# Optimization experiments

Hardware: AMD Instinct MI355X
Metric: run time of the kernel (lower is better)

## Reference

```python
import jax, jax.numpy as jnp
import numpy as np

B, T, C = 4, 2048, 512
H, CDR_HEADS = 8, 2
D = C // H


def setup_inputs() -> dict:
    key = jax.random.key(0)
    ks = jax.random.split(key, 12)
    s = 1.0 / np.sqrt(C)
    return {
        "x": jax.random.normal(ks[0], (B, T, C), dtype=jnp.float32),
        "mask": jax.random.randint(ks[1], (B, T), 0, 2, dtype=jnp.int32),
        "cdrs_score": jax.random.randint(ks[2], (B, T), 0, 2, dtype=jnp.int32),
        "Wq": jax.random.normal(ks[3], (C, C), dtype=jnp.float32) * s,
        "bq": jnp.zeros((C,), dtype=jnp.float32),
        "Wk": jax.random.normal(ks[4], (C, C), dtype=jnp.float32) * s,
        "bk": jnp.zeros((C,), dtype=jnp.float32),
        "Wv": jax.random.normal(ks[5], (C, C), dtype=jnp.float32) * s,
        "bv": jnp.zeros((C,), dtype=jnp.float32),
        "Wo": jax.random.normal(ks[6], (C, C), dtype=jnp.float32) * s,
        "bo": jnp.zeros((C,), dtype=jnp.float32),
    }


def reference(x, mask, cdrs_score, Wq, bq, Wk, bk, Wv, bv, Wo, bo):
    # projections -> [B, H, T, D]
    def heads(y):
        return y.reshape(B, T, H, D).transpose(0, 2, 1, 3)

    q = heads(x @ Wq + bq)
    k = heads(x @ Wk + bk)
    v = heads(x @ Wv + bv)

    scores = jnp.einsum("bhqd,bhkd->bhqk", q, k) / jnp.sqrt(jnp.float32(D))

    # padding mask: keys with mask==0 are invalid for all heads
    pad = (mask == 0)[:, None, None, :]                      # [B,1,1,T]
    scores = jnp.where(pad, -jnp.inf, scores)

    # CDR key mask for the first CDR_HEADS heads; disabled if a sample has no CDR tokens
    cdr_key_mask = (cdrs_score == 0)                          # [B, T]
    all_masked = jnp.all(cdr_key_mask, axis=-1, keepdims=True)  # [B, 1]
    cdr_key_mask = jnp.where(all_masked, False, cdr_key_mask)   # [B, T]
    head_is_cdr = (jnp.arange(H) < CDR_HEADS)[None, :, None, None]  # [1,H,1,1]
    cdr_full = head_is_cdr & cdr_key_mask[:, None, None, :]         # [B,H,1,T]
    scores = jnp.where(cdr_full, -jnp.inf, scores)

    attn = jax.nn.softmax(scores, axis=-1)                    # [B,H,T,T]
    ctx = jnp.einsum("bhqk,bhkd->bhqd", attn, v)
    ctx = ctx.transpose(0, 2, 1, 3).reshape(B, T, C)
    return ctx @ Wo + bo
```

## Files before the change

kernel.cpp:

```cpp
#include <hip/hip_runtime.h>
#include <math.h>

#define B_ 4
#define T_ 2048
#define C_ 512
#define H_ 8
#define D_ 64
#define CDR_HEADS_ 2
#define NROWS (B_ * T_)

typedef unsigned short ush;
typedef __bf16  bf16x8 __attribute__((ext_vector_type(8)));
typedef float   f32x4  __attribute__((ext_vector_type(4)));

#define MFMA16(a, b, c) __builtin_amdgcn_mfma_f32_16x16x32_bf16((a), (b), (c), 0, 0, 0)

static __device__ __forceinline__ ush f2bf(float f) {
    unsigned u = __float_as_uint(f);
    u += 0x7FFF + ((u >> 16) & 1);
    return (ush)(u >> 16);
}
static __device__ __forceinline__ float bf2f(ush h) {
    return __uint_as_float(((unsigned)h) << 16);
}

static __device__ __forceinline__ void gload16(const void* gsrc, void* ldst) {
    __builtin_amdgcn_global_load_lds(
        (const __attribute__((address_space(1))) unsigned int*)gsrc,
        (__attribute__((address_space(3))) unsigned int*)ldst, 16, 0, 0);
}

__global__ __launch_bounds__(256) void prep_kernel(
    const float* __restrict__ x,
    const float* __restrict__ W0, const float* __restrict__ W1,
    const float* __restrict__ W2, const float* __restrict__ W3,
    const int* __restrict__ mask, const int* __restrict__ cdrs,
    ush* __restrict__ Xh, ush* __restrict__ Xl,
    ush* __restrict__ Wth, ush* __restrict__ Wtl,
    int* __restrict__ klist, int* __restrict__ kcnt) {
    __shared__ int s_any;
    __shared__ int sa[256], sb[256];
    const int bid = blockIdx.x, tid = threadIdx.x;

    if (bid < 2048) {
        const int id = bid * 256 + tid;
        const int m = id >> 6, kc = id & 63;
        const float* p = x + (size_t)m * C_ + kc * 8;
        const float4 a = ((const float4*)p)[0];
        const float4 b2 = ((const float4*)p)[1];
        float xv[8] = {a.x, a.y, a.z, a.w, b2.x, b2.y, b2.z, b2.w};
        union { ush u[8]; int4 q; } hi, lo;
#pragma unroll
        for (int i = 0; i < 8; ++i) {
            const ush h = f2bf(xv[i]);
            hi.u[i] = h;
            lo.u[i] = f2bf(xv[i] - bf2f(h));
        }
        const int mt = m >> 7, ml = m & 127, kt = kc >> 2, cidx = kc & 3;
        const size_t tbase = ((size_t)mt * 16 + kt) * 4096;
        const int boff = ml * 64 + ((cidx ^ ((ml >> 1) & 3)) << 4);
        *(int4*)((char*)(Xh + tbase) + boff) = hi.q;
        *(int4*)((char*)(Xl + tbase) + boff) = lo.q;
    } else if (bid < 2560) {
        const int z = bid - 2048;
        const int mat = z >> 7;
        const float* W = (mat == 0) ? W0 : (mat == 1) ? W1 : (mat == 2) ? W2 : W3;
        const int id = (z & 127) * 256 + tid;
        const int n = id & 511, kc = id >> 9;
        float xv[8];
#pragma unroll
        for (int j = 0; j < 8; ++j)
            xv[j] = W[(size_t)(kc * 8 + j) * C_ + n];
        union { ush u[8]; int4 q; } hi, lo;
#pragma unroll
        for (int i = 0; i < 8; ++i) {
            const ush h = f2bf(xv[i]);
            hi.u[i] = h;
            lo.u[i] = f2bf(xv[i] - bf2f(h));
        }
        const int nt = n >> 7, nl = n & 127, kt = kc >> 2, cidx = kc & 3;
        const size_t tbase = (size_t)mat * 262144 + ((size_t)nt * 16 + kt) * 4096;
        const int boff = nl * 64 + ((cidx ^ ((nl >> 1) & 3)) << 4);
        *(int4*)((char*)(Wth + tbase) + boff) = hi.q;
        *(int4*)((char*)(Wtl + tbase) + boff) = lo.q;
    } else {
        const int b = bid - 2560;
        if (tid == 0) s_any = 0;
        __syncthreads();
        int m8[8], c8[8];
        int any = 0, ca = 0;
        const int base = b * T_ + tid * 8;
#pragma unroll
        for (int i = 0; i < 8; ++i) {
            m8[i] = mask[base + i];
            c8[i] = cdrs[base + i];
            any |= c8[i];
            ca += (m8[i] != 0);
        }
        if (any) s_any = 1;
        __syncthreads();
        const int en = s_any;
        int cb = 0;
#pragma unroll
        for (int i = 0; i < 8; ++i)
            cb += (m8[i] != 0 && (!en || c8[i] != 0));
        sa[tid] = ca; sb[tid] = cb;
        __syncthreads();
        for (int off = 1; off < 256; off <<= 1) {
            int va = 0, vb = 0;
            if (tid >= off) { va = sa[tid - off]; vb = sb[tid - off]; }
            __syncthreads();
            sa[tid] += va; sb[tid] += vb;
            __syncthreads();
        }
        int offA = sa[tid] - ca;
        int offB = sb[tid] - cb;
        int* la = klist + (size_t)(b * 2 + 0) * T_;
        int* lb = klist + (size_t)(b * 2 + 1) * T_;
#pragma unroll
        for (int i = 0; i < 8; ++i) {
            const int t = tid * 8 + i;
            if (m8[i] != 0) la[offA++] = t;
            if (m8[i] != 0 && (!en || c8[i] != 0)) lb[offB++] = t;
        }
        if (tid == 255) {
            kcnt[b * 2 + 0] = sa[255];
            kcnt[b * 2 + 1] = sb[255];
        }
    }
}

template <int OUTMODE>
static __device__ __forceinline__ void gemm3_body(
    const ush* __restrict__ Ah_g, const ush* __restrict__ Al_g,
    const ush* __restrict__ Bh_g, const ush* __restrict__ Bl_g,
    const float* __restrict__ bias, void* __restrict__ outp, float scale) {
    __shared__ char lds[32768];
    char* const sAh = lds;
    char* const sAl = lds + 8192;
    char* const sBh = lds + 16384;
    char* const sBl = lds + 24576;

    const int tid = threadIdx.x;
    const int lane = tid & 63, w = tid >> 6;
    const int g = lane >> 4, l15 = lane & 15;
    const int wr = w >> 1, wc = w & 1;
    const int mt = blockIdx.x, nt = blockIdx.y;

    const char* gAh = (const char*)Ah_g + (size_t)(mt * 16) * 8192;
    const char* gAl = (const char*)Al_g + (size_t)(mt * 16) * 8192;
    const char* gBh = (const char*)Bh_g + (size_t)(nt * 16) * 8192;
    const char* gBl = (const char*)Bl_g + (size_t)(nt * 16) * 8192;

    f32x4 acc[4][4];
#pragma unroll
    for (int i = 0; i < 4; ++i)
#pragma unroll
        for (int j = 0; j < 4; ++j)
#pragma unroll
            for (int r = 0; r < 4; ++r) acc[i][j][r] = 0.f;

    const int lw = w * 2048;
    for (int kt = 0; kt < 16; ++kt) {
        __syncthreads();
        const size_t gb = (size_t)kt * 8192 + lw + lane * 16;
        gload16(gAh + gb,        sAh + lw);
        gload16(gAh + gb + 1024, sAh + lw + 1024);
        gload16(gAl + gb,        sAl + lw);
        gload16(gAl + gb + 1024, sAl + lw + 1024);
        gload16(gBh + gb,        sBh + lw);
        gload16(gBh + gb + 1024, sBh + lw + 1024);
        gload16(gBl + gb,        sBl + lw);
        gload16(gBl + gb + 1024, sBl + lw + 1024);
        __syncthreads();

        bf16x8 fah[4], fal[4], fbh[4], fbl[4];
#pragma unroll
        for (int rb = 0; rb < 4; ++rb) {
            const int row = wr * 64 + rb * 16 + l15;
            const int off = row * 64 + ((g ^ ((row >> 1) & 3)) << 4);
            fah[rb] = __builtin_bit_cast(bf16x8, *(const int4*)(sAh + off));
            fal[rb] = __builtin_bit_cast(bf16x8, *(const int4*)(sAl + off));
        }
#pragma unroll
        for (int cb = 0; cb < 4; ++cb) {
            const int row = wc * 64 + cb * 16 + l15;
            const int off = row * 64 + ((g ^ ((row >> 1) & 3)) << 4);
            fbh[cb] = __builtin_bit_cast(bf16x8, *(const int4*)(sBh + off));
            fbl[cb] = __builtin_bit_cast(bf16x8, *(const int4*)(sBl + off));
        }
#pragma unroll
        for (int rb = 0; rb < 4; ++rb)
#pragma unroll
            for (int cb = 0; cb < 4; ++cb) {
                acc[rb][cb] = MFMA16(fah[rb], fbh[cb], acc[rb][cb]);
                acc[rb][cb] = MFMA16(fah[rb], fbl[cb], acc[rb][cb]);
                acc[rb][cb] = MFMA16(fal[rb], fbh[cb], acc[rb][cb]);
            }
    }

    const int mbase = mt * 128 + wr * 64;
    const int nbase = nt * 128 + wc * 64;
    float bcol[4];
#pragma unroll
    for (int cb = 0; cb < 4; ++cb) bcol[cb] = bias[nbase + cb * 16 + l15];

#pragma unroll
    for (int rb = 0; rb < 4; ++rb)
#pragma unroll
        for (int cb = 0; cb < 4; ++cb) {
            const int colg = nbase + cb * 16 + l15;
#pragma unroll
            for (int r = 0; r < 4; ++r) {
                const int m = mbase + rb * 16 + g * 4 + r;
                const float vv = acc[rb][cb][r] + bcol[cb];
                if (OUTMODE == 0) {
                    ((float*)outp)[(size_t)m * C_ + colg] = vv;
                } else {
                    const int bb = m >> 11, t = m & (T_ - 1);
                    const int h = colg >> 6, d = colg & 63;
                    ((ush*)outp)[(((size_t)(bb * H_ + h) * T_ + t) * D_) + d] =
                        f2bf(vv * scale);
                }
            }
        }
}

__global__ __launch_bounds__(256) void gemm3_qkv_kernel(
    const ush* __restrict__ Xh, const ush* __restrict__ Xl,
    const ush* __restrict__ Wth, const ush* __restrict__ Wtl,
    const float* __restrict__ bq, const float* __restrict__ bk,
    const float* __restrict__ bv,
    ush* __restrict__ Qb, ush* __restrict__ Kb, ush* __restrict__ Vb) {
    const int z = blockIdx.z;
    const ush* bh = Wth + (size_t)z * 262144;
    const ush* bl = Wtl + (size_t)z * 262144;
    if (z == 0)      gemm3_body<1>(Xh, Xl, bh, bl, bq, Qb, 0.125f);
    else if (z == 1) gemm3_body<1>(Xh, Xl, bh, bl, bk, Kb, 1.0f);
    else             gemm3_body<1>(Xh, Xl, bh, bl, bv, Vb, 1.0f);
}

__global__ __launch_bounds__(256) void gemm3_out_kernel(
    const ush* __restrict__ Ch, const ush* __restrict__ Cl,
    const ush* __restrict__ Wth, const ush* __restrict__ Wtl,
    const float* __restrict__ bo, float* __restrict__ out) {
    gemm3_body<0>(Ch, Cl, Wth + (size_t)3 * 262144, Wtl + (size_t)3 * 262144,
                  bo, out, 1.0f);
}

__global__ __launch_bounds__(256) void gather_kernel(
    const ush* __restrict__ Kb, const ush* __restrict__ Vb,
    const int* __restrict__ klist, const int* __restrict__ kcnt,
    ush* __restrict__ Kc, ush* __restrict__ Vct) {
    __shared__ ush Vs[64 * 72];
    const int tid = threadIdx.x;
    const int ti = blockIdx.x, h = blockIdx.y, b = blockIdx.z;
    const int sel = (h < CDR_HEADS_) ? 1 : 0;
    const int NV = kcnt[b * 2 + sel];
    if (ti * 64 >= NV) return;
    const int* __restrict__ list = klist + (size_t)(b * 2 + sel) * T_;
    const size_t bh = (size_t)b * H_ + h;
    const ush* kb_ = Kb + bh * T_ * D_;
    const ush* vb_ = Vb + bh * T_ * D_;
    ush* kt = Kc + bh * (32 * 4096) + (size_t)ti * 4096;
    ush* vt = Vct + bh * (32 * 4096) + (size_t)ti * 4096;

    const int i = tid >> 2, c = tid & 3;
    const int pos = ti * 64 + i;
    int4 kv0 = {0,0,0,0}, kv1 = {0,0,0,0}, vv0 = {0,0,0,0}, vv1 = {0,0,0,0};
    if (pos < NV) {
        const int row = list[pos];
        const int4* kr = (const int4*)(kb_ + (size_t)row * D_ + c * 16);
        kv0 = kr[0]; kv1 = kr[1];
        const int4* vr = (const int4*)(vb_ + (size_t)row * D_ + c * 16);
        vv0 = vr[0]; vv1 = vr[1];
    }
    {
        const int s0 = (c * 2) ^ (i & 7), s1 = (c * 2 + 1) ^ (i & 7);
        *(int4*)(kt + i * 64 + s0 * 8) = kv0;
        *(int4*)(kt + i * 64 + s1 * 8) = kv1;
    }
    *(int4*)(Vs + i * 72 + c * 16)     = vv0;
    *(int4*)(Vs + i * 72 + c * 16 + 8) = vv1;
    __syncthreads();
    {
        const int d = tid >> 2, c2 = tid & 3;
        union { ush u[16]; int4 q[2]; } pk;
#pragma unroll
        for (int ii = 0; ii < 16; ++ii)
            pk.u[ii] = Vs[(c2 * 16 + ii) * 72 + d];
        const int s0 = (c2 * 2) ^ (d & 7), s1 = (c2 * 2 + 1) ^ (d & 7);
        *(int4*)(vt + d * 64 + s0 * 8) = pk.q[0];
        *(int4*)(vt + d * 64 + s1 * 8) = pk.q[1];
    }
}

__global__ __launch_bounds__(512) void attn_mfma_kernel(
    const ush* __restrict__ Qb, const ush* __restrict__ Kc,
    const ush* __restrict__ Vct, const int* __restrict__ kcnt,
    ush* __restrict__ Xh, ush* __restrict__ Xl) {
    __shared__ ush Ks[2][4096];
    __shared__ ush Vts[2][4096];
    __shared__ ush Pl[8192];

    const int tid = threadIdx.x;
    const int lane = tid & 63, w = tid >> 6;
    const int g = lane >> 4, l15 = lane & 15;

    const int i = blockIdx.x;
    const int x7 = i & 7, local = i >> 3;
    const int b = local >> 4;
    const int h = (x7 - 2 * b) & 7;
    const int qt = local & 15;
    const int bh = b * H_ + h;

    const int sel = (h < CDR_HEADS_) ? 1 : 0;
    const int NV = kcnt[b * 2 + sel];
    const int ntiles = (NV + 63) >> 6;
    const int swz = (l15 & 7) << 4;

    bf16x8 aq[2];
    {
        const ush* qp = Qb + ((size_t)bh * T_ + qt * 128 + w * 16) * D_;
#pragma unroll
        for (int kc = 0; kc < 2; ++kc)
            aq[kc] = __builtin_bit_cast(bf16x8,
                *(const int4*)(qp + l15 * D_ + kc * 32 + g * 8));
    }

    f32x4 cacc[4];
#pragma unroll
    for (int db = 0; db < 4; ++db)
#pragma unroll
        for (int r = 0; r < 4; ++r) cacc[db][r] = 0.f;
    float mr = -INFINITY, lr = 0.f;

    const char* ktiles = (const char*)(Kc + (size_t)bh * (32 * 4096));
    const char* vtiles = (const char*)(Vct + (size_t)bh * (32 * 4096));
    char* Pw = (char*)Pl + w * 2048;
    const int lwo = w * 512;

    gload16(ktiles + lwo * 2 + lane * 16, &Ks[0][lwo]);
    gload16(vtiles + lwo * 2 + lane * 16, &Vts[0][lwo]);
    __syncthreads();

    for (int t = 0; t < ntiles; ++t) {
        const int cur = t & 1, nxt = cur ^ 1;
        if (t + 1 < ntiles) {
            gload16(ktiles + (size_t)(t + 1) * 8192 + lwo * 2 + lane * 16,
                    &Ks[nxt][lwo]);
            gload16(vtiles + (size_t)(t + 1) * 8192 + lwo * 2 + lane * 16,
                    &Vts[nxt][lwo]);
        }

        bf16x8 bk[4][2];
#pragma unroll
        for (int j = 0; j < 4; ++j) {
            const int rowb = (j * 16 + l15) * 128;
            bk[j][0] = __builtin_bit_cast(bf16x8,
                *(const int4*)((const char*)Ks[cur] + ((rowb + g * 16) ^ swz)));
            bk[j][1] = __builtin_bit_cast(bf16x8,
                *(const int4*)((const char*)Ks[cur] + ((rowb + 64 + g * 16) ^ swz)));
        }
        f32x4 s[4];
        const f32x4 z4 = {0.f, 0.f, 0.f, 0.f};
        __builtin_amdgcn_s_setprio(1);
#pragma unroll
        for (int j = 0; j < 4; ++j) s[j] = MFMA16(bk[j][0], aq[0], z4);
#pragma unroll
        for (int j = 0; j < 4; ++j) s[j] = MFMA16(bk[j][1], aq[1], s[j]);
        __builtin_amdgcn_s_setprio(0);

        const int kb0 = t * 64;
        if (kb0 + 64 > NV) {
#pragma unroll
            for (int j = 0; j < 4; ++j)
#pragma unroll
                for (int r = 0; r < 4; ++r)
                    if (kb0 + j * 16 + g * 4 + r >= NV) s[j][r] = -INFINITY;
        }

        float pmax = s[0][0];
#pragma unroll
        for (int j = 0; j < 4; ++j)
#pragma unroll
            for (int r = 0; r < 4; ++r) pmax = fmaxf(pmax, s[j][r]);
        pmax = fmaxf(pmax, __shfl_xor(pmax, 16));
        pmax = fmaxf(pmax, __shfl_xor(pmax, 32));
        if (!__all(pmax <= mr + 8.f)) {
            const float mn = fmaxf(mr, pmax);
            const float rr = __expf(mr - mn);
            mr = mn;
            lr *= rr;
#pragma unroll
            for (int r = 0; r < 4; ++r) {
                const float rrq = __shfl(rr, g * 4 + r, 16);
#pragma unroll
                for (int db = 0; db < 4; ++db) cacc[db][r] *= rrq;
            }
        }
        float sum = 0.f;
#pragma unroll
        for (int j = 0; j < 4; ++j)
#pragma unroll
            for (int r = 0; r < 4; ++r) {
                const float p = __expf(s[j][r] - mr);
                s[j][r] = p;
                sum += p;
            }
        sum += __shfl_xor(sum, 16);
        sum += __shfl_xor(sum, 32);
        lr += sum;

#pragma unroll
        for (int j = 0; j < 4; ++j) {
            const ush u0 = __builtin_bit_cast(ush, (__bf16)s[j][0]);
            const ush u1 = __builtin_bit_cast(ush, (__bf16)s[j][1]);
            const ush u2 = __builtin_bit_cast(ush, (__bf16)s[j][2]);
            const ush u3 = __builtin_bit_cast(ush, (__bf16)s[j][3]);
            uint2 pk;
            pk.x = (unsigned)u0 | ((unsigned)u1 << 16);
            pk.y = (unsigned)u2 | ((unsigned)u3 << 16);
            const int sb = (j * 2 + (g >> 1)) ^ (l15 & 7);
            *(uint2*)(Pw + l15 * 128 + sb * 16 + (g & 1) * 8) = pk;
        }

        bf16x8 pa[2];
#pragma unroll
        for (int kc = 0; kc < 2; ++kc)
            pa[kc] = __builtin_bit_cast(bf16x8,
                *(const int4*)(Pw + l15 * 128 + (((kc * 4 + g) ^ (l15 & 7)) << 4)));
        __builtin_amdgcn_s_setprio(1);
#pragma unroll
        for (int kc = 0; kc < 2; ++kc)
#pragma unroll
            for (int db = 0; db < 4; ++db) {
                bf16x8 vbf = __builtin_bit_cast(bf16x8,
                    *(const int4*)((const char*)Vts[cur] +
                        ((((db * 16 + l15) * 128) + kc * 64 + g * 16) ^ swz)));
                cacc[db] = MFMA16(pa[kc], vbf, cacc[db]);
            }
        __builtin_amdgcn_s_setprio(0);

        __syncthreads();
    }

    const int mt = b * 16 + qt;
#pragma unroll
    for (int r = 0; r < 4; ++r) {
        const float lrq = __shfl(lr, g * 4 + r, 16);
        const float inv = 1.f / lrq;
        const int ml = w * 16 + g * 4 + r;
#pragma unroll
        for (int db = 0; db < 4; ++db) {
            const int col = h * 64 + db * 16 + l15;
            const float val = cacc[db][r] * inv;
            const __bf16 hb = (__bf16)val;
            const __bf16 lb2 = (__bf16)(val - (float)hb);
            const int kt2 = col >> 5;
            const int cidx = (col >> 3) & 3;
            const size_t tb = ((size_t)mt * 16 + kt2) * 4096;
            const int boff = ml * 64 + ((cidx ^ ((ml >> 1) & 3)) << 4) + (l15 & 7) * 2;
            *(ush*)((char*)(Xh + tb) + boff) = __builtin_bit_cast(ush, hb);
            *(ush*)((char*)(Xl + tb) + boff) = __builtin_bit_cast(ush, lb2);
        }
    }
}

extern "C" void kernel_launch(void* const* d_in, const int* in_sizes, int n_in,
                              void* d_out, int out_size, void* d_ws, size_t ws_size,
                              hipStream_t stream) {
    const float* x    = (const float*)d_in[0];
    const int*   mask = (const int*)d_in[1];
    const int*   cdrs = (const int*)d_in[2];
    const float* Wq   = (const float*)d_in[3];
    const float* bq   = (const float*)d_in[4];
    const float* Wk   = (const float*)d_in[5];
    const float* bk   = (const float*)d_in[6];
    const float* Wv   = (const float*)d_in[7];
    const float* bv   = (const float*)d_in[8];
    const float* Wo   = (const float*)d_in[9];
    const float* bo   = (const float*)d_in[10];
    float* out = (float*)d_out;

    const size_t per = (size_t)B_ * H_ * T_ * D_;
    ush* Qb  = (ush*)d_ws;
    ush* Kb  = Qb + per;
    ush* Vb  = Kb + per;
    ush* Kc  = Vb + per;
    ush* Vct = Kc + per;
    ush* Xh  = Vct + per;
    ush* Xl  = Xh + per;
    ush* Wth = Xl + per;
    ush* Wtl = Wth + 4 * 262144;
    int* klist = (int*)(Wtl + 4 * 262144);
    int* kcnt  = klist + (size_t)B_ * 2 * T_;

    prep_kernel<<<2564, 256, 0, stream>>>(x, Wq, Wk, Wv, Wo, mask, cdrs,
                                          Xh, Xl, Wth, Wtl, klist, kcnt);

    gemm3_qkv_kernel<<<dim3(64, 4, 3), 256, 0, stream>>>(
        Xh, Xl, Wth, Wtl, bq, bk, bv, Qb, Kb, Vb);

    gather_kernel<<<dim3(32, H_, B_), 256, 0, stream>>>(Kb, Vb, klist, kcnt,
                                                        Kc, Vct);

    attn_mfma_kernel<<<512, 512, 0, stream>>>(Qb, Kc, Vct, kcnt, Xh, Xl);

    gemm3_out_kernel<<<dim3(64, 4), 256, 0, stream>>>(Xh, Xl, Wth, Wtl, bo, out);
}
```

Measured before the change: 198.5 us.

## Fuse K/V gather into QKV GEMM epilogue and double-buffer GEMM LDS

The prep kernel now writes per-token compacted positions instead of key lists. The K and V GEMM epilogues scatter results straight into the compacted, swizzled Kc/Vct layouts, which removes the separate gather kernel and the Kb/Vb round trip through global memory. The shared GEMM body also double-buffers its LDS tiles, raises wave priority around the MFMA block, and remaps block IDs across XCDs. The costs are scattered 2-byte stores, doubled LDS use that may lower occupancy, and padding rows of the last key tile that are no longer zero-filled.

Result: faster. 191.0 us (-3.8%).

```diff
diff --git a/kernel.cpp b/kernel.cpp
--- a/kernel.cpp
+++ b/kernel.cpp
@@ -37,7 +37,7 @@
     const int* __restrict__ mask, const int* __restrict__ cdrs,
     ush* __restrict__ Xh, ush* __restrict__ Xl,
     ush* __restrict__ Wth, ush* __restrict__ Wtl,
-    int* __restrict__ klist, int* __restrict__ kcnt) {
+    int* __restrict__ posA, int* __restrict__ posB, int* __restrict__ kcnt) {
     __shared__ int s_any;
     __shared__ int sa[256], sb[256];
     const int bid = blockIdx.x, tid = threadIdx.x;
@@ -115,13 +115,13 @@
         }
         int offA = sa[tid] - ca;
         int offB = sb[tid] - cb;
-        int* la = klist + (size_t)(b * 2 + 0) * T_;
-        int* lb = klist + (size_t)(b * 2 + 1) * T_;
 #pragma unroll
         for (int i = 0; i < 8; ++i) {
             const int t = tid * 8 + i;
-            if (m8[i] != 0) la[offA++] = t;
-            if (m8[i] != 0 && (!en || c8[i] != 0)) lb[offB++] = t;
+            const bool av = (m8[i] != 0);
+            const bool bv = av && (!en || c8[i] != 0);
+            posA[b * T_ + t] = av ? offA++ : -1;
+            posB[b * T_ + t] = bv ? offB++ : -1;
         }
         if (tid == 255) {
             kcnt[b * 2 + 0] = sa[255];
@@ -132,26 +132,25 @@
 
 template <int OUTMODE>
 static __device__ __forceinline__ void gemm3_body(
+    char* __restrict__ lds0, char* __restrict__ lds1,
+    int mt, int nt,
     const ush* __restrict__ Ah_g, const ush* __restrict__ Al_g,
     const ush* __restrict__ Bh_g, const ush* __restrict__ Bl_g,
-    const float* __restrict__ bias, void* __restrict__ outp, float scale) {
-    __shared__ char lds[32768];
-    char* const sAh = lds;
-    char* const sAl = lds + 8192;
-    char* const sBh = lds + 16384;
-    char* const sBl = lds + 24576;
-
+    const float* __restrict__ bias, void* __restrict__ outp, float scale,
+    const int* __restrict__ posA, const int* __restrict__ posB,
+    ush* __restrict__ Kc, ush* __restrict__ Vct) {
     const int tid = threadIdx.x;
     const int lane = tid & 63, w = tid >> 6;
     const int g = lane >> 4, l15 = lane & 15;
     const int wr = w >> 1, wc = w & 1;
-    const int mt = blockIdx.x, nt = blockIdx.y;
 
     const char* gAh = (const char*)Ah_g + (size_t)(mt * 16) * 8192;
     const char* gAl = (const char*)Al_g + (size_t)(mt * 16) * 8192;
     const char* gBh = (const char*)Bh_g + (size_t)(nt * 16) * 8192;
     const char* gBl = (const char*)Bl_g + (size_t)(nt * 16) * 8192;
 
+    const int lw = w * 2048;
+
     f32x4 acc[4][4];
 #pragma unroll
     for (int i = 0; i < 4; ++i)
@@ -160,35 +159,42 @@
 #pragma unroll
             for (int r = 0; r < 4; ++r) acc[i][j][r] = 0.f;
 
-    const int lw = w * 2048;
+    auto stage = [&](char* s, int kt) {
+        const size_t gb = (size_t)kt * 8192 + lw + lane * 16;
+        gload16(gAh + gb,        s + lw);
+        gload16(gAh + gb + 1024, s + lw + 1024);
+        gload16(gAl + gb,        s + 8192 + lw);
+        gload16(gAl + gb + 1024, s + 8192 + lw + 1024);
+        gload16(gBh + gb,        s + 16384 + lw);
+        gload16(gBh + gb + 1024, s + 16384 + lw + 1024);
+        gload16(gBl + gb,        s + 24576 + lw);
+        gload16(gBl + gb + 1024, s + 24576 + lw + 1024);
+    };
+
+    stage(lds0, 0);
+    __syncthreads();
+
     for (int kt = 0; kt < 16; ++kt) {
-        __syncthreads();
-        const size_t gb = (size_t)kt * 8192 + lw + lane * 16;
-        gload16(gAh + gb,        sAh + lw);
-        gload16(gAh + gb + 1024, sAh + lw + 1024);
-        gload16(gAl + gb,        sAl + lw);
-        gload16(gAl + gb + 1024, sAl + lw + 1024);
-        gload16(gBh + gb,        sBh + lw);
-        gload16(gBh + gb + 1024, sBh + lw + 1024);
-        gload16(gBl + gb,        sBl + lw);
-        gload16(gBl + gb + 1024, sBl + lw + 1024);
-        __syncthreads();
+        char* s  = (kt & 1) ? lds1 : lds0;
+        char* sn = (kt & 1) ? lds0 : lds1;
+        if (kt + 1 < 16) stage(sn, kt + 1);
 
         bf16x8 fah[4], fal[4], fbh[4], fbl[4];
 #pragma unroll
         for (int rb = 0; rb < 4; ++rb) {
             const int row = wr * 64 + rb * 16 + l15;
             const int off = row * 64 + ((g ^ ((row >> 1) & 3)) << 4);
-            fah[rb] = __builtin_bit_cast(bf16x8, *(const int4*)(sAh + off));
-            fal[rb] = __builtin_bit_cast(bf16x8, *(const int4*)(sAl + off));
+            fah[rb] = __builtin_bit_cast(bf16x8, *(const int4*)(s + off));
+            fal[rb] = __builtin_bit_cast(bf16x8, *(const int4*)(s + 8192 + off));
         }
 #pragma unroll
         for (int cb = 0; cb < 4; ++cb) {
             const int row = wc * 64 + cb * 16 + l15;
             const int off = row * 64 + ((g ^ ((row >> 1) & 3)) << 4);
-            fbh[cb] = __builtin_bit_cast(bf16x8, *(const int4*)(sBh + off));
-            fbl[cb] = __builtin_bit_cast(bf16x8, *(const int4*)(sBl + off));
-        }
+            fbh[cb] = __builtin_bit_cast(bf16x8, *(const int4*)(s + 16384 + off));
+            fbl[cb] = __builtin_bit_cast(bf16x8, *(const int4*)(s + 24576 + off));
+        }
+        __builtin_amdgcn_s_setprio(1);
 #pragma unroll
         for (int rb = 0; rb < 4; ++rb)
 #pragma unroll
@@ -197,6 +203,8 @@
                 acc[rb][cb] = MFMA16(fah[rb], fbl[cb], acc[rb][cb]);
                 acc[rb][cb] = MFMA16(fal[rb], fbh[cb], acc[rb][cb]);
             }
+        __builtin_amdgcn_s_setprio(0);
+        __syncthreads();
     }
 
     const int mbase = mt * 128 + wr * 64;
@@ -216,11 +224,28 @@
                 const float vv = acc[rb][cb][r] + bcol[cb];
                 if (OUTMODE == 0) {
                     ((float*)outp)[(size_t)m * C_ + colg] = vv;
-                } else {
+                } else if (OUTMODE == 1) {
                     const int bb = m >> 11, t = m & (T_ - 1);
                     const int h = colg >> 6, d = colg & 63;
                     ((ush*)outp)[(((size_t)(bb * H_ + h) * T_ + t) * D_) + d] =
                         f2bf(vv * scale);
+                } else {
+                    const int bb = m >> 11, t = m & (T_ - 1);
+                    const int h = colg >> 6, d = colg & 63;
+                    const int pos = (h < CDR_HEADS_ ? posB : posA)[bb * T_ + t];
+                    if (pos >= 0) {
+                        char* base = (char*)(OUTMODE == 2 ? Kc : Vct) +
+                                     (size_t)(bb * H_ + h) * 262144 +
+                                     (size_t)(pos >> 6) * 8192;
+                        const int i = pos & 63;
+                        const ush val = f2bf(vv);
+                        if (OUTMODE == 2)
+                            *(ush*)(base + i * 128 + (((d >> 3) ^ (i & 7)) << 4) +
+                                    (d & 7) * 2) = val;
+                        else
+                            *(ush*)(base + d * 128 + (((i >> 3) ^ (d & 7)) << 4) +
+                                    (i & 7) * 2) = val;
+                    }
                 }
             }
         }
@@ -230,69 +255,36 @@
     const ush* __restrict__ Xh, const ush* __restrict__ Xl,
     const ush* __restrict__ Wth, const ush* __restrict__ Wtl,
     const float* __restrict__ bq, const float* __restrict__ bk,
-    const float* __restrict__ bv,
-    ush* __restrict__ Qb, ush* __restrict__ Kb, ush* __restrict__ Vb) {
-    const int z = blockIdx.z;
+    const float* __restrict__ bv, ush* __restrict__ Qb,
+    const int* __restrict__ posA, const int* __restrict__ posB,
+    ush* __restrict__ Kc, ush* __restrict__ Vct) {
+    __shared__ char lds[2][32768];
+    const int wg = (blockIdx.x & 7) * 96 + (blockIdx.x >> 3);
+    const int mt = wg / 12, sub = wg % 12;
+    const int nt = sub & 3, z = sub >> 2;
     const ush* bh = Wth + (size_t)z * 262144;
     const ush* bl = Wtl + (size_t)z * 262144;
-    if (z == 0)      gemm3_body<1>(Xh, Xl, bh, bl, bq, Qb, 0.125f);
-    else if (z == 1) gemm3_body<1>(Xh, Xl, bh, bl, bk, Kb, 1.0f);
-    else             gemm3_body<1>(Xh, Xl, bh, bl, bv, Vb, 1.0f);
+    if (z == 0)
+        gemm3_body<1>(lds[0], lds[1], mt, nt, Xh, Xl, bh, bl, bq, Qb, 0.125f,
+                      nullptr, nullptr, nullptr, nullptr);
+    else if (z == 1)
+        gemm3_body<2>(lds[0], lds[1], mt, nt, Xh, Xl, bh, bl, bk, nullptr, 1.0f,
+                      posA, posB, Kc, Vct);
+    else
+        gemm3_body<3>(lds[0], lds[1], mt, nt, Xh, Xl, bh, bl, bv, nullptr, 1.0f,
+                      posA, posB, Kc, Vct);
 }
 
 __global__ __launch_bounds__(256) void gemm3_out_kernel(
     const ush* __restrict__ Ch, const ush* __restrict__ Cl,
     const ush* __restrict__ Wth, const ush* __restrict__ Wtl,
     const float* __restrict__ bo, float* __restrict__ out) {
-    gemm3_body<0>(Ch, Cl, Wth + (size_t)3 * 262144, Wtl + (size_t)3 * 262144,
-                  bo, out, 1.0f);
-}
-
-__global__ __launch_bounds__(256) void gather_kernel(
-    const ush* __restrict__ Kb, const ush* __restrict__ Vb,
-    const int* __restrict__ klist, const int* __restrict__ kcnt,
-    ush* __restrict__ Kc, ush* __restrict__ Vct) {
-    __shared__ ush Vs[64 * 72];
-    const int tid = threadIdx.x;
-    const int ti = blockIdx.x, h = blockIdx.y, b = blockIdx.z;
-    const int sel = (h < CDR_HEADS_) ? 1 : 0;
-    const int NV = kcnt[b * 2 + sel];
-    if (ti * 64 >= NV) return;
-    const int* __restrict__ list = klist + (size_t)(b * 2 + sel) * T_;
-    const size_t bh = (size_t)b * H_ + h;
-    const ush* kb_ = Kb + bh * T_ * D_;
-    const ush* vb_ = Vb + bh * T_ * D_;
-    ush* kt = Kc + bh * (32 * 4096) + (size_t)ti * 4096;
-    ush* vt = Vct + bh * (32 * 4096) + (size_t)ti * 4096;
-
-    const int i = tid >> 2, c = tid & 3;
-    const int pos = ti * 64 + i;
-    int4 kv0 = {0,0,0,0}, kv1 = {0,0,0,0}, vv0 = {0,0,0,0}, vv1 = {0,0,0,0};
-    if (pos < NV) {
-        const int row = list[pos];
-        const int4* kr = (const int4*)(kb_ + (size_t)row * D_ + c * 16);
-        kv0 = kr[0]; kv1 = kr[1];
-        const int4* vr = (const int4*)(vb_ + (size_t)row * D_ + c * 16);
-        vv0 = vr[0]; vv1 = vr[1];
-    }
-    {
-        const int s0 = (c * 2) ^ (i & 7), s1 = (c * 2 + 1) ^ (i & 7);
-        *(int4*)(kt + i * 64 + s0 * 8) = kv0;
-        *(int4*)(kt + i * 64 + s1 * 8) = kv1;
-    }
-    *(int4*)(Vs + i * 72 + c * 16)     = vv0;
-    *(int4*)(Vs + i * 72 + c * 16 + 8) = vv1;
-    __syncthreads();
-    {
-        const int d = tid >> 2, c2 = tid & 3;
-        union { ush u[16]; int4 q[2]; } pk;
-#pragma unroll
-        for (int ii = 0; ii < 16; ++ii)
-            pk.u[ii] = Vs[(c2 * 16 + ii) * 72 + d];
-        const int s0 = (c2 * 2) ^ (d & 7), s1 = (c2 * 2 + 1) ^ (d & 7);
-        *(int4*)(vt + d * 64 + s0 * 8) = pk.q[0];
-        *(int4*)(vt + d * 64 + s1 * 8) = pk.q[1];
-    }
+    __shared__ char lds[2][32768];
+    const int wg = (blockIdx.x & 7) * 32 + (blockIdx.x >> 3);
+    const int mt = wg >> 2, nt = wg & 3;
+    gemm3_body<0>(lds[0], lds[1], mt, nt, Ch, Cl, Wth + (size_t)3 * 262144,
+                  Wtl + (size_t)3 * 262144, bo, out, 1.0f,
+                  nullptr, nullptr, nullptr, nullptr);
 }
 
 __global__ __launch_bounds__(512) void attn_mfma_kernel(
@@ -485,27 +477,23 @@
 
     const size_t per = (size_t)B_ * H_ * T_ * D_;
     ush* Qb  = (ush*)d_ws;
-    ush* Kb  = Qb + per;
-    ush* Vb  = Kb + per;
-    ush* Kc  = Vb + per;
+    ush* Kc  = Qb + per;
     ush* Vct = Kc + per;
     ush* Xh  = Vct + per;
     ush* Xl  = Xh + per;
     ush* Wth = Xl + per;
     ush* Wtl = Wth + 4 * 262144;
-    int* klist = (int*)(Wtl + 4 * 262144);
-    int* kcnt  = klist + (size_t)B_ * 2 * T_;
+    int* posA = (int*)(Wtl + 4 * 262144);
+    int* posB = posA + NROWS;
+    int* kcnt = posB + NROWS;
 
     prep_kernel<<<2564, 256, 0, stream>>>(x, Wq, Wk, Wv, Wo, mask, cdrs,
-                                          Xh, Xl, Wth, Wtl, klist, kcnt);
-
-    gemm3_qkv_kernel<<<dim3(64, 4, 3), 256, 0, stream>>>(
-        Xh, Xl, Wth, Wtl, bq, bk, bv, Qb, Kb, Vb);
-
-    gather_kernel<<<dim3(32, H_, B_), 256, 0, stream>>>(Kb, Vb, klist, kcnt,
-                                                        Kc, Vct);
+                                          Xh, Xl, Wth, Wtl, posA, posB, kcnt);
+
+    gemm3_qkv_kernel<<<768, 256, 0, stream>>>(
+        Xh, Xl, Wth, Wtl, bq, bk, bv, Qb, posA, posB, Kc, Vct);
 
     attn_mfma_kernel<<<512, 512, 0, stream>>>(Qb, Kc, Vct, kcnt, Xh, Xl);
 
-    gemm3_out_kernel<<<dim3(64, 4), 256, 0, stream>>>(Xh, Xl, Wth, Wtl, bo, out);
-}
+    gemm3_out_kernel<<<256, 256, 0, stream>>>(Xh, Xl, Wth, Wtl, bo, out);
+}
```
